# Performance work log

Hardware: AMD Instinct MI355X
Metric: run time of the kernel (lower is better)

## Reference

```python
import jax, jax.numpy as jnp
import numpy as np

SEQ_LEN = 1024
BATCH = 256
HIDDEN = 100
OUT = 1

L_FILTER = [-0.0106, 0.0329, 0.0308, -0.187, -0.028, 0.6309, 0.7148, 0.2304]
H_FILTER = [-0.2304, 0.7148, -0.6309, -0.028, 0.187, 0.0308, -0.0329, -0.0106]


def _create_W(P, is_l, rng):
    filt = L_FILTER if is_l else H_FILTER
    eps = np.min(np.abs(filt))
    W = rng.standard_normal((P, P)) * 0.1 * eps
    for i in range(P):
        for k, j in enumerate(range(i, min(i + len(filt), P))):
            W[i, j] = filt[k]
    return jnp.asarray(W, dtype=jnp.float32)


def setup_inputs() -> dict:
    key = jax.random.key(0)
    ks = jax.random.split(key, 16)
    rng = np.random.default_rng(0)
    T, H = SEQ_LEN, HIDDEN
    s = 1.0 / np.sqrt(H)

    def lstm_params(k):
        k1, k2, k3 = jax.random.split(k, 3)
        Wih = jax.random.uniform(k1, (4 * H, 1), jnp.float32, -s, s)
        Whh = jax.random.uniform(k2, (4 * H, H), jnp.float32, -s, s)
        b = jax.random.uniform(k3, (4 * H,), jnp.float32, -s, s)
        return Wih, Whh, b

    Wih1, Whh1, b1 = lstm_params(ks[0])
    Wih2, Whh2, b2 = lstm_params(ks[1])
    Wih3, Whh3, b3 = lstm_params(ks[2])
    return {
        "x": jax.random.normal(ks[3], (BATCH, T, 1), jnp.float32),
        "W1H": _create_W(T, False, rng),
        "b1H": jax.random.uniform(ks[4], (T,), jnp.float32, -1 / np.sqrt(T), 1 / np.sqrt(T)),
        "W1L": _create_W(T, True, rng),
        "b1L": jax.random.uniform(ks[5], (T,), jnp.float32, -1 / np.sqrt(T), 1 / np.sqrt(T)),
        "W2H": _create_W(T // 2, False, rng),
        "b2H": jax.random.uniform(ks[6], (T // 2,), jnp.float32, -1 / np.sqrt(T // 2), 1 / np.sqrt(T // 2)),
        "W2L": _create_W(T // 2, True, rng),
        "b2L": jax.random.uniform(ks[7], (T // 2,), jnp.float32, -1 / np.sqrt(T // 2), 1 / np.sqrt(T // 2)),
        "Wih1": Wih1, "Whh1": Whh1, "b1": b1,
        "Wih2": Wih2, "Whh2": Whh2, "b2": b2,
        "Wih3": Wih3, "Whh3": Whh3, "b3": b3,
        "Wout": jax.random.uniform(ks[8], (OUT, H), jnp.float32, -s, s),
        "bout": jax.random.uniform(ks[9], (OUT,), jnp.float32, -s, s),
    }


def _avgpool2(x):  # [B, L] -> [B, L//2], AvgPool1d(kernel=2, stride=2)
    B, L = x.shape
    return x.reshape(B, L // 2, 2).mean(-1)


def _lstm(x, Wih, Whh, b):
    # x: [B, T, 1]; torch LSTM gate order i, f, g, o; h0 = c0 = 0
    H = Whh.shape[1]
    gx = jnp.einsum('bti,gi->btg', x, Wih) + b  # [B, T, 4H]

    def step(carry, g):
        h, c = carry
        z = g + h @ Whh.T
        i, f, gg, o = jnp.split(z, 4, axis=-1)
        c = jax.nn.sigmoid(f) * c + jax.nn.sigmoid(i) * jnp.tanh(gg)
        h = jax.nn.sigmoid(o) * jnp.tanh(c)
        return (h, c), h

    B = x.shape[0]
    h0 = jnp.zeros((B, H), x.dtype)
    _, hs = jax.lax.scan(step, (h0, h0), jnp.swapaxes(gx, 0, 1))
    return jnp.swapaxes(hs, 0, 1)  # [B, T, H]


def reference(x, W1H, b1H, W1L, b1L, W2H, b2H, W2L, b2L,
              Wih1, Whh1, b1, Wih2, Whh2, b2, Wih3, Whh3, b3, Wout, bout):
    inp = x[:, :, -1]  # [B, T]
    ah1 = jax.nn.sigmoid(inp @ W1H.T + b1H)
    al1 = jax.nn.sigmoid(inp @ W1L.T + b1L)
    xh1 = _avgpool2(ah1)  # [B, T/2]
    xl1 = _avgpool2(al1)  # [B, T/2]
    ah2 = jax.nn.sigmoid(xl1 @ W2H.T + b2H)
    al2 = jax.nn.sigmoid(xl1 @ W2L.T + b2L)
    xh2 = _avgpool2(ah2)  # [B, T/4]
    xl2 = _avgpool2(al2)  # [B, T/4]
    s1 = _lstm(xh1[..., None], Wih1, Whh1, b1)
    s2 = _lstm(xh2[..., None], Wih2, Whh2, b2)
    s3 = _lstm(xl2[..., None], Wih3, Whh3, b3)
    cat = jnp.concatenate([s1, s2, s3], axis=1)  # [B, T, H]
    out = cat @ Wout.T + bout  # [B, T, OUT]
    return out[:, -1, :]
```

## Files before the change

kernel.cpp:

```cpp
#include <hip/hip_runtime.h>
#include <math.h>

typedef __bf16 bf16x8 __attribute__((ext_vector_type(8)));
typedef _Float16 f16x8 __attribute__((ext_vector_type(8)));
typedef _Float16 f16x4 __attribute__((ext_vector_type(4)));
typedef float f32x4 __attribute__((ext_vector_type(4)));

__device__ __forceinline__ unsigned short f2bf(float f) {
  unsigned int u = __builtin_bit_cast(unsigned int, f);
  u += 0x7fffu + ((u >> 16) & 1u);
  return (unsigned short)(u >> 16);
}
__device__ __forceinline__ unsigned int pack2bf(float a, float b) {
  return (unsigned int)f2bf(a) | ((unsigned int)f2bf(b) << 16);
}

#define GK_PADK 40
template <int WFP32, int XFP32>
__global__ __launch_bounds__(256) void gemm_mfma_sig_pool(
    const void* __restrict__ Wv, const float* __restrict__ bias,
    const void* __restrict__ Xv, void* __restrict__ Y,
    int K, int Np, int out_bf16) {
  __shared__ unsigned short Wt[64][GK_PADK];
  __shared__ unsigned short Xt[64][GK_PADK];
  const int tid = threadIdx.x;
  const int i_base = blockIdx.x * 64;
  const int b_base = blockIdx.y * 64;
  const int srow = tid >> 2, sseg = tid & 3;
  const int wv = tid >> 6, lane = tid & 63;
  const int wn = wv & 1, wb = wv >> 1;
  const int L15 = lane & 15, q = lane >> 4;

  f32x4 acc[2][2] = {};
  for (int k0 = 0; k0 < K; k0 += 32) {
    if (WFP32) {
      const float* Wf = (const float*)Wv;
      const float4 a = *(const float4*)&Wf[(size_t)(i_base + srow) * K + k0 + sseg * 8];
      const float4 b = *(const float4*)&Wf[(size_t)(i_base + srow) * K + k0 + sseg * 8 + 4];
      uint4 p = { pack2bf(a.x, a.y), pack2bf(a.z, a.w), pack2bf(b.x, b.y), pack2bf(b.z, b.w) };
      *(uint4*)&Wt[srow][sseg * 8] = p;
    } else {
      *(uint4*)&Wt[srow][sseg * 8] =
          *(const uint4*)&((const unsigned short*)Wv)[(size_t)(i_base + srow) * K + k0 + sseg * 8];
    }
    if (XFP32) {
      const float* Xf = (const float*)Xv;
      const float4 a = *(const float4*)&Xf[(size_t)(b_base + srow) * K + k0 + sseg * 8];
      const float4 b = *(const float4*)&Xf[(size_t)(b_base + srow) * K + k0 + sseg * 8 + 4];
      uint4 p = { pack2bf(a.x, a.y), pack2bf(a.z, a.w), pack2bf(b.x, b.y), pack2bf(b.z, b.w) };
      *(uint4*)&Xt[srow][sseg * 8] = p;
    } else {
      *(uint4*)&Xt[srow][sseg * 8] =
          *(const uint4*)&((const unsigned short*)Xv)[(size_t)(b_base + srow) * K + k0 + sseg * 8];
    }
    __syncthreads();
    bf16x8 a0 = *(const bf16x8*)&Wt[wn * 32 + L15][q * 8];
    bf16x8 a1 = *(const bf16x8*)&Wt[wn * 32 + 16 + L15][q * 8];
    bf16x8 b0 = *(const bf16x8*)&Xt[wb * 32 + L15][q * 8];
    bf16x8 b1 = *(const bf16x8*)&Xt[wb * 32 + 16 + L15][q * 8];
    acc[0][0] = __builtin_amdgcn_mfma_f32_16x16x32_bf16(a0, b0, acc[0][0], 0, 0, 0);
    acc[0][1] = __builtin_amdgcn_mfma_f32_16x16x32_bf16(a0, b1, acc[0][1], 0, 0, 0);
    acc[1][0] = __builtin_amdgcn_mfma_f32_16x16x32_bf16(a1, b0, acc[1][0], 0, 0, 0);
    acc[1][1] = __builtin_amdgcn_mfma_f32_16x16x32_bf16(a1, b1, acc[1][1], 0, 0, 0);
    __syncthreads();
  }

  const int nb0 = i_base + wn * 32;
  const int bc0 = b_base + wb * 32 + L15;
#pragma unroll
  for (int mg = 0; mg < 2; mg++) {
    const int nrow = nb0 + mg * 16 + q * 4;
    const float bi0 = bias[nrow], bi1 = bias[nrow + 1];
    const float bi2 = bias[nrow + 2], bi3 = bias[nrow + 3];
#pragma unroll
    for (int bg = 0; bg < 2; bg++) {
      const int b = bc0 + bg * 16;
      f32x4 A = acc[mg][bg];
      const float a0 = __builtin_amdgcn_rcpf(1.f + __expf(-(A[0] + bi0)));
      const float a1 = __builtin_amdgcn_rcpf(1.f + __expf(-(A[1] + bi1)));
      const float a2 = __builtin_amdgcn_rcpf(1.f + __expf(-(A[2] + bi2)));
      const float a3 = __builtin_amdgcn_rcpf(1.f + __expf(-(A[3] + bi3)));
      const float p0 = 0.5f * (a0 + a1), p1 = 0.5f * (a2 + a3);
      const int pidx = nrow >> 1;
      if (out_bf16) {
        *(unsigned int*)&((unsigned short*)Y)[(size_t)b * Np + pidx] = pack2bf(p0, p1);
      } else {
        *(float2*)&((float*)Y)[(size_t)b * Np + pidx] = make_float2(p0, p1);
      }
    }
  }
}

__global__ __launch_bounds__(256) void prep_whh(
    const float* __restrict__ Whh, const float* __restrict__ b3,
    _Float16* __restrict__ P) {
  const int idx = blockIdx.x * 256 + threadIdx.x;
  if (idx >= 400 * 16) return;
  const int row = idx >> 4, ch = idx & 15;
  const int hid = row >> 2, gate = row & 3;
  const int src = gate * 100 + hid;
  f16x8 v;
#pragma unroll
  for (int j = 0; j < 8; j++) {
    const int k = ch * 8 + j;
    float f = 0.f;
    if (k < 100) f = Whh[(size_t)src * 100 + k];
    v[j] = (_Float16)f;
  }
  *(f16x8*)&P[(size_t)row * 128 + ch * 8] = v;
}

#define TSTEPS 256

__device__ __forceinline__ float qb0(float x) {
  return __builtin_bit_cast(float, __builtin_amdgcn_mov_dpp(__builtin_bit_cast(int, x), 0x00, 0xf, 0xf, true));
}
__device__ __forceinline__ float qb1(float x) {
  return __builtin_bit_cast(float, __builtin_amdgcn_mov_dpp(__builtin_bit_cast(int, x), 0x55, 0xf, 0xf, true));
}
__device__ __forceinline__ float qb2(float x) {
  return __builtin_bit_cast(float, __builtin_amdgcn_mov_dpp(__builtin_bit_cast(int, x), 0xAA, 0xf, 0xf, true));
}
__device__ __forceinline__ float qb3(float x) {
  return __builtin_bit_cast(float, __builtin_amdgcn_mov_dpp(__builtin_bit_cast(int, x), 0xFF, 0xf, 0xf, true));
}

__global__ __launch_bounds__(512, 2) void lstm_mfma(
    const float* __restrict__ X, const _Float16* __restrict__ P,
    const float* __restrict__ Whh, const float* __restrict__ Wih,
    const float* __restrict__ b3, const float* __restrict__ Wout,
    const float* __restrict__ bout, float* __restrict__ out) {
  const int bat = blockIdx.x;
  const int t = threadIdx.x;
  const int w = t >> 6, lane = t & 63;
  const int quad = lane >> 4, c = lane & 15;
  const int TB = (w == 7) ? 21 : w * 3;
  const int NT = (w == 7) ? 4 : 3;

  __shared__ __align__(16) _Float16 hbuf[2][128];
  __shared__ float xrow[TSTEPS];
  __shared__ float red[128];

  for (int i = t; i < TSTEPS; i += 512) xrow[i] = X[(size_t)bat * TSTEPS + i];
  if (t < 128) { hbuf[0][t] = (_Float16)0.f; hbuf[1][t] = (_Float16)0.f; }

#define LDA(J, KT) const f16x8 A##J##KT = \
    *(const f16x8*)&P[(size_t)((TB + J) * 16 + c) * 128 + (KT) * 32 + quad * 8];
  LDA(0,0) LDA(0,1) LDA(0,2)
  LDA(1,0) LDA(1,1) LDA(1,2)
  LDA(2,0) LDA(2,1) LDA(2,2)
  LDA(3,0) LDA(3,1) LDA(3,2)
#undef LDA

  const bool act = (c < 4 * NT);
  const int J = c >> 2, g = c & 3;
  const int myhid = 4 * (TB + (act ? J : 0)) + quad;
  const int grow = g * 100 + myhid;
  const float u_ = Wih[grow];
  const float bz = b3[grow];
  const float4 wt = *(const float4*)&Whh[(size_t)grow * 100 + 96];
  const float kk = (g == 2) ? 2.f : 1.f;
  const float mm = (g == 2) ? 2.f : 1.f;
  const float dd = (g == 2) ? -1.f : 0.f;
  float cst = 0.f;
  __syncthreads();

#define SIG(zz) __builtin_amdgcn_rcpf(1.f + __expf(-(zz)))
#define STEPB(HC, HN, XT)                                                      \
  {                                                                            \
    const _Float16* hc = (HC);                                                 \
    const f16x8 B0 = *(const f16x8*)&hc[0 * 32 + quad * 8];                    \
    const f16x8 B1 = *(const f16x8*)&hc[1 * 32 + quad * 8];                    \
    const f16x8 B2 = *(const f16x8*)&hc[2 * 32 + quad * 8];                    \
    f32x4 z0 = {0.f,0.f,0.f,0.f}, z1 = z0, z2 = z0, z3 = z0;                   \
    { f32x4 za = z0, zb = z0;                                                  \
      za = __builtin_amdgcn_mfma_f32_16x16x32_f16(A00, B0, za, 0, 0, 0);       \
      zb = __builtin_amdgcn_mfma_f32_16x16x32_f16(A01, B1, zb, 0, 0, 0);       \
      za = __builtin_amdgcn_mfma_f32_16x16x32_f16(A02, B2, za, 0, 0, 0);       \
      z0 = za + zb; }                                                          \
    { f32x4 za = {0.f,0.f,0.f,0.f}, zb = za;                                   \
      za = __builtin_amdgcn_mfma_f32_16x16x32_f16(A10, B0, za, 0, 0, 0);       \
      zb = __builtin_amdgcn_mfma_f32_16x16x32_f16(A11, B1, zb, 0, 0, 0);       \
      za = __builtin_amdgcn_mfma_f32_16x16x32_f16(A12, B2, za, 0, 0, 0);       \
      z1 = za + zb; }                                                          \
    { f32x4 za = {0.f,0.f,0.f,0.f}, zb = za;                                   \
      za = __builtin_amdgcn_mfma_f32_16x16x32_f16(A20, B0, za, 0, 0, 0);       \
      zb = __builtin_amdgcn_mfma_f32_16x16x32_f16(A21, B1, zb, 0, 0, 0);       \
      za = __builtin_amdgcn_mfma_f32_16x16x32_f16(A22, B2, za, 0, 0, 0);       \
      z2 = za + zb; }                                                          \
    if (w == 7) {                                                              \
      f32x4 za = {0.f,0.f,0.f,0.f}, zb = za;                                   \
      za = __builtin_amdgcn_mfma_f32_16x16x32_f16(A30, B0, za, 0, 0, 0);       \
      zb = __builtin_amdgcn_mfma_f32_16x16x32_f16(A31, B1, zb, 0, 0, 0);       \
      za = __builtin_amdgcn_mfma_f32_16x16x32_f16(A32, B2, za, 0, 0, 0);       \
      z3 = za + zb; }                                                          \
    if (act) {                                                                 \
      const f32x4 zt = (J == 0) ? z0 : (J == 1) ? z1 : (J == 2) ? z2 : z3;     \
      float zs = (g == 0) ? zt[0] : (g == 1) ? zt[1] : (g == 2) ? zt[2] : zt[3];\
      const f16x4 ht = *(const f16x4*)&hc[96];                                 \
      zs = fmaf(wt.x, (float)ht[0], zs);                                       \
      zs = fmaf(wt.y, (float)ht[1], zs);                                       \
      zs = fmaf(wt.z, (float)ht[2], zs);                                       \
      zs = fmaf(wt.w, (float)ht[3], zs);                                       \
      zs = fmaf(u_, (XT), zs + bz);                                            \
      const float a = mm * SIG(kk * zs) + dd;                                  \
      const float ai = qb0(a), af = qb1(a), ag = qb2(a), ao = qb3(a);          \
      cst = fmaf(af, cst, ai * ag);                                            \
      const float th = 2.f * SIG(2.f * cst) - 1.f;                             \
      if (g == 0) (HN)[myhid] = (_Float16)(ao * th);                           \
    }                                                                          \
    __syncthreads();                                                           \
  }

  for (int step = 0; step < TSTEPS; step += 2) {
    STEPB(hbuf[0], hbuf[1], xrow[step]);
    STEPB(hbuf[1], hbuf[0], xrow[step + 1]);
  }
#undef STEPB
#undef SIG

  if (t < 128) {
    float a = 0.f;
    if (t < 100) a = (float)hbuf[0][t] * Wout[t];
    red[t] = a;
  }
  __syncthreads();
  if (t == 0) {
    float s = 0.f;
#pragma unroll
    for (int k = 0; k < 128; k++) s += red[k];
    out[bat] = s + bout[0];
  }
}

extern "C" void kernel_launch(void* const* d_in, const int* in_sizes, int n_in,
                              void* d_out, int out_size, void* d_ws, size_t ws_size,
                              hipStream_t stream) {
  const float* x    = (const float*)d_in[0];
  const float* W1L  = (const float*)d_in[3];
  const float* b1L  = (const float*)d_in[4];
  const float* W2L  = (const float*)d_in[7];
  const float* b2L  = (const float*)d_in[8];
  const float* Wih3 = (const float*)d_in[15];
  const float* Whh3 = (const float*)d_in[16];
  const float* b3   = (const float*)d_in[17];
  const float* Wout = (const float*)d_in[18];
  const float* bout = (const float*)d_in[19];
  float* out = (float*)d_out;

  unsigned short* xl1b = (unsigned short*)d_ws;
  float* xl2 = (float*)(xl1b + (size_t)256 * 512);
  _Float16* P = (_Float16*)(xl2 + (size_t)256 * 256);

  prep_whh<<<25, 256, 0, stream>>>(Whh3, b3, P);
  gemm_mfma_sig_pool<1, 1><<<dim3(16, 4), 256, 0, stream>>>(W1L, b1L, x, xl1b, 1024, 512, 1);
  gemm_mfma_sig_pool<1, 0><<<dim3(8, 4), 256, 0, stream>>>(W2L, b2L, xl1b, xl2, 512, 256, 0);
  lstm_mfma<<<256, 512, 0, stream>>>(xl2, P, Whh3, Wih3, b3, Wout, bout, out);
}
```

Baseline: 264.6 us.

## Halve LSTM block to four waves and pre-convert GEMM inputs to bf16

The LSTM recurrence kernel now runs each batch row with 256 threads (4 waves) instead of 512. Each wave computes 6–7 MFMA tiles and each lane handles two hidden-unit cell states, which cuts the cost of the per-step block barrier. The old Whh prep kernel is merged into a new conversion kernel that also casts W1L, W2L and x to bf16, so both GEMMs read bf16 operands directly. The trade-off is longer serial per-wave work per step and an extra full pass over the weights on every call.

```diff
diff --git a/kernel.cpp b/kernel.cpp
--- a/kernel.cpp
+++ b/kernel.cpp
@@ -13,6 +13,40 @@
 }
 __device__ __forceinline__ unsigned int pack2bf(float a, float b) {
   return (unsigned int)f2bf(a) | ((unsigned int)f2bf(b) << 16);
+}
+
+__global__ __launch_bounds__(256) void convert_prep(
+    const float* __restrict__ s0, const float* __restrict__ s1,
+    const float* __restrict__ s2, unsigned short* __restrict__ d0,
+    unsigned short* __restrict__ d1, unsigned short* __restrict__ d2,
+    int n0, int n1, int n2,
+    const float* __restrict__ Whh, _Float16* __restrict__ P) {
+  const int b = blockIdx.x;
+  if (b < 1536) {
+    int i4 = (b * 256 + threadIdx.x) * 4;
+    const float* s; unsigned short* d; int off;
+    if (i4 < n0) { s = s0; d = d0; off = i4; }
+    else if (i4 < n0 + n1) { s = s1; d = d1; off = i4 - n0; }
+    else if (i4 < n0 + n1 + n2) { s = s2; d = d2; off = i4 - n0 - n1; }
+    else return;
+    float4 v = *(const float4*)&s[off];
+    ushort4 o = { f2bf(v.x), f2bf(v.y), f2bf(v.z), f2bf(v.w) };
+    *(ushort4*)&d[off] = o;
+  } else {
+    const int idx = (b - 1536) * 256 + threadIdx.x;
+    if (idx >= 400 * 16) return;
+    const int row = idx >> 4, ch = idx & 15;
+    const int hid = row >> 2, gate = row & 3;
+    const int src = gate * 100 + hid;
+    f16x8 v;
+#pragma unroll
+    for (int j = 0; j < 8; j++) {
+      const int k = ch * 8 + j;
+      float f = (k < 100) ? Whh[(size_t)src * 100 + k] : 0.f;
+      v[j] = (_Float16)f;
+    }
+    *(f16x8*)&P[(size_t)row * 128 + ch * 8] = v;
+  }
 }
 
 #define GK_PADK 40
@@ -91,25 +125,6 @@
   }
 }
 
-__global__ __launch_bounds__(256) void prep_whh(
-    const float* __restrict__ Whh, const float* __restrict__ b3,
-    _Float16* __restrict__ P) {
-  const int idx = blockIdx.x * 256 + threadIdx.x;
-  if (idx >= 400 * 16) return;
-  const int row = idx >> 4, ch = idx & 15;
-  const int hid = row >> 2, gate = row & 3;
-  const int src = gate * 100 + hid;
-  f16x8 v;
-#pragma unroll
-  for (int j = 0; j < 8; j++) {
-    const int k = ch * 8 + j;
-    float f = 0.f;
-    if (k < 100) f = Whh[(size_t)src * 100 + k];
-    v[j] = (_Float16)f;
-  }
-  *(f16x8*)&P[(size_t)row * 128 + ch * 8] = v;
-}
-
 #define TSTEPS 256
 
 __device__ __forceinline__ float qb0(float x) {
@@ -125,7 +140,7 @@
   return __builtin_bit_cast(float, __builtin_amdgcn_mov_dpp(__builtin_bit_cast(int, x), 0xFF, 0xf, 0xf, true));
 }
 
-__global__ __launch_bounds__(512, 2) void lstm_mfma(
+__global__ __launch_bounds__(256, 1) void lstm_mfma(
     const float* __restrict__ X, const _Float16* __restrict__ P,
     const float* __restrict__ Whh, const float* __restrict__ Wih,
     const float* __restrict__ b3, const float* __restrict__ Wout,
@@ -134,15 +149,15 @@
   const int t = threadIdx.x;
   const int w = t >> 6, lane = t & 63;
   const int quad = lane >> 4, c = lane & 15;
-  const int TB = (w == 7) ? 21 : w * 3;
-  const int NT = (w == 7) ? 4 : 3;
+  const int TB = (w == 3) ? 18 : w * 6;
+  const int NT = (w == 3) ? 7 : 6;
 
   __shared__ __align__(16) _Float16 hbuf[2][128];
   __shared__ float xrow[TSTEPS];
   __shared__ float red[128];
 
-  for (int i = t; i < TSTEPS; i += 512) xrow[i] = X[(size_t)bat * TSTEPS + i];
-  if (t < 128) { hbuf[0][t] = (_Float16)0.f; hbuf[1][t] = (_Float16)0.f; }
+  for (int i = t; i < TSTEPS; i += 256) xrow[i] = X[(size_t)bat * TSTEPS + i];
+  ((_Float16*)hbuf)[t] = (_Float16)0.f;
 
 #define LDA(J, KT) const f16x8 A##J##KT = \
     *(const f16x8*)&P[(size_t)((TB + J) * 16 + c) * 128 + (KT) * 32 + quad * 8];
@@ -150,19 +165,26 @@
   LDA(1,0) LDA(1,1) LDA(1,2)
   LDA(2,0) LDA(2,1) LDA(2,2)
   LDA(3,0) LDA(3,1) LDA(3,2)
+  LDA(4,0) LDA(4,1) LDA(4,2)
+  LDA(5,0) LDA(5,1) LDA(5,2)
+  LDA(6,0) LDA(6,1) LDA(6,2)
 #undef LDA
 
-  const bool act = (c < 4 * NT);
-  const int J = c >> 2, g = c & 3;
-  const int myhid = 4 * (TB + (act ? J : 0)) + quad;
-  const int grow = g * 100 + myhid;
-  const float u_ = Wih[grow];
-  const float bz = b3[grow];
-  const float4 wt = *(const float4*)&Whh[(size_t)grow * 100 + 96];
+  const int g = c & 3, ssel = c >> 2;
+  const int sB = 4 + ssel;
+  const bool actB = (sB < NT);
+  const int hidA = 4 * (TB + ssel) + quad;
+  const int hidB = 4 * (TB + (actB ? sB : 0)) + quad;
+  const int growA = g * 100 + hidA;
+  const int growB = g * 100 + hidB;
+  const float uA = Wih[growA], bzA = b3[growA];
+  const float uB = Wih[growB], bzB = b3[growB];
+  const float4 wtA = *(const float4*)&Whh[(size_t)growA * 100 + 96];
+  const float4 wtB = *(const float4*)&Whh[(size_t)growB * 100 + 96];
   const float kk = (g == 2) ? 2.f : 1.f;
   const float mm = (g == 2) ? 2.f : 1.f;
   const float dd = (g == 2) ? -1.f : 0.f;
-  float cst = 0.f;
+  float cstA = 0.f, cstB = 0.f;
   __syncthreads();
 
 #define SIG(zz) __builtin_amdgcn_rcpf(1.f + __expf(-(zz)))
@@ -173,41 +195,58 @@
     const f16x8 B1 = *(const f16x8*)&hc[1 * 32 + quad * 8];                    \
     const f16x8 B2 = *(const f16x8*)&hc[2 * 32 + quad * 8];                    \
     f32x4 z0 = {0.f,0.f,0.f,0.f}, z1 = z0, z2 = z0, z3 = z0;                   \
-    { f32x4 za = z0, zb = z0;                                                  \
-      za = __builtin_amdgcn_mfma_f32_16x16x32_f16(A00, B0, za, 0, 0, 0);       \
-      zb = __builtin_amdgcn_mfma_f32_16x16x32_f16(A01, B1, zb, 0, 0, 0);       \
-      za = __builtin_amdgcn_mfma_f32_16x16x32_f16(A02, B2, za, 0, 0, 0);       \
-      z0 = za + zb; }                                                          \
-    { f32x4 za = {0.f,0.f,0.f,0.f}, zb = za;                                   \
-      za = __builtin_amdgcn_mfma_f32_16x16x32_f16(A10, B0, za, 0, 0, 0);       \
-      zb = __builtin_amdgcn_mfma_f32_16x16x32_f16(A11, B1, zb, 0, 0, 0);       \
-      za = __builtin_amdgcn_mfma_f32_16x16x32_f16(A12, B2, za, 0, 0, 0);       \
-      z1 = za + zb; }                                                          \
-    { f32x4 za = {0.f,0.f,0.f,0.f}, zb = za;                                   \
-      za = __builtin_amdgcn_mfma_f32_16x16x32_f16(A20, B0, za, 0, 0, 0);       \
-      zb = __builtin_amdgcn_mfma_f32_16x16x32_f16(A21, B1, zb, 0, 0, 0);       \
-      za = __builtin_amdgcn_mfma_f32_16x16x32_f16(A22, B2, za, 0, 0, 0);       \
-      z2 = za + zb; }                                                          \
-    if (w == 7) {                                                              \
-      f32x4 za = {0.f,0.f,0.f,0.f}, zb = za;                                   \
-      za = __builtin_amdgcn_mfma_f32_16x16x32_f16(A30, B0, za, 0, 0, 0);       \
-      zb = __builtin_amdgcn_mfma_f32_16x16x32_f16(A31, B1, zb, 0, 0, 0);       \
-      za = __builtin_amdgcn_mfma_f32_16x16x32_f16(A32, B2, za, 0, 0, 0);       \
-      z3 = za + zb; }                                                          \
-    if (act) {                                                                 \
-      const f32x4 zt = (J == 0) ? z0 : (J == 1) ? z1 : (J == 2) ? z2 : z3;     \
-      float zs = (g == 0) ? zt[0] : (g == 1) ? zt[1] : (g == 2) ? zt[2] : zt[3];\
-      const f16x4 ht = *(const f16x4*)&hc[96];                                 \
-      zs = fmaf(wt.x, (float)ht[0], zs);                                       \
-      zs = fmaf(wt.y, (float)ht[1], zs);                                       \
-      zs = fmaf(wt.z, (float)ht[2], zs);                                       \
-      zs = fmaf(wt.w, (float)ht[3], zs);                                       \
-      zs = fmaf(u_, (XT), zs + bz);                                            \
-      const float a = mm * SIG(kk * zs) + dd;                                  \
-      const float ai = qb0(a), af = qb1(a), ag = qb2(a), ao = qb3(a);          \
-      cst = fmaf(af, cst, ai * ag);                                            \
-      const float th = 2.f * SIG(2.f * cst) - 1.f;                             \
-      if (g == 0) (HN)[myhid] = (_Float16)(ao * th);                           \
+    f32x4 z4 = z0, z5 = z0, z6 = z0;                                           \
+    z0 = __builtin_amdgcn_mfma_f32_16x16x32_f16(A00, B0, z0, 0, 0, 0);         \
+    z0 = __builtin_amdgcn_mfma_f32_16x16x32_f16(A01, B1, z0, 0, 0, 0);         \
+    z0 = __builtin_amdgcn_mfma_f32_16x16x32_f16(A02, B2, z0, 0, 0, 0);         \
+    z1 = __builtin_amdgcn_mfma_f32_16x16x32_f16(A10, B0, z1, 0, 0, 0);         \
+    z1 = __builtin_amdgcn_mfma_f32_16x16x32_f16(A11, B1, z1, 0, 0, 0);         \
+    z1 = __builtin_amdgcn_mfma_f32_16x16x32_f16(A12, B2, z1, 0, 0, 0);         \
+    z2 = __builtin_amdgcn_mfma_f32_16x16x32_f16(A20, B0, z2, 0, 0, 0);         \
+    z2 = __builtin_amdgcn_mfma_f32_16x16x32_f16(A21, B1, z2, 0, 0, 0);         \
+    z2 = __builtin_amdgcn_mfma_f32_16x16x32_f16(A22, B2, z2, 0, 0, 0);         \
+    z3 = __builtin_amdgcn_mfma_f32_16x16x32_f16(A30, B0, z3, 0, 0, 0);         \
+    z3 = __builtin_amdgcn_mfma_f32_16x16x32_f16(A31, B1, z3, 0, 0, 0);         \
+    z3 = __builtin_amdgcn_mfma_f32_16x16x32_f16(A32, B2, z3, 0, 0, 0);         \
+    z4 = __builtin_amdgcn_mfma_f32_16x16x32_f16(A40, B0, z4, 0, 0, 0);         \
+    z4 = __builtin_amdgcn_mfma_f32_16x16x32_f16(A41, B1, z4, 0, 0, 0);         \
+    z4 = __builtin_amdgcn_mfma_f32_16x16x32_f16(A42, B2, z4, 0, 0, 0);         \
+    z5 = __builtin_amdgcn_mfma_f32_16x16x32_f16(A50, B0, z5, 0, 0, 0);         \
+    z5 = __builtin_amdgcn_mfma_f32_16x16x32_f16(A51, B1, z5, 0, 0, 0);         \
+    z5 = __builtin_amdgcn_mfma_f32_16x16x32_f16(A52, B2, z5, 0, 0, 0);         \
+    if (w == 3) {                                                              \
+      z6 = __builtin_amdgcn_mfma_f32_16x16x32_f16(A60, B0, z6, 0, 0, 0);       \
+      z6 = __builtin_amdgcn_mfma_f32_16x16x32_f16(A61, B1, z6, 0, 0, 0);       \
+      z6 = __builtin_amdgcn_mfma_f32_16x16x32_f16(A62, B2, z6, 0, 0, 0);       \
+    }                                                                          \
+    const f16x4 htv = *(const f16x4*)&hc[96];                                  \
+    const float h96 = (float)htv[0], h97 = (float)htv[1];                      \
+    const float h98 = (float)htv[2], h99 = (float)htv[3];                      \
+    const f32x4 ztA = (ssel == 0) ? z0 : (ssel == 1) ? z1 : (ssel == 2) ? z2 : z3; \
+    const f32x4 ztB = (ssel == 0) ? z4 : (ssel == 1) ? z5 : z6;                \
+    float zsA = (g == 0) ? ztA[0] : (g == 1) ? ztA[1] : (g == 2) ? ztA[2] : ztA[3]; \
+    float zsB = (g == 0) ? ztB[0] : (g == 1) ? ztB[1] : (g == 2) ? ztB[2] : ztB[3]; \
+    {                                                                          \
+      float zz = zsA;                                                          \
+      zz = fmaf(wtA.x, h96, zz); zz = fmaf(wtA.y, h97, zz);                    \
+      zz = fmaf(wtA.z, h98, zz); zz = fmaf(wtA.w, h99, zz);                    \
+      zz = fmaf(uA, (XT), zz + bzA);                                           \
+      const float a = mm * SIG(kk * zz) + dd;                                  \
+      const float ai = qb0(a), af = qb1(a), ag2 = qb2(a), ao = qb3(a);         \
+      cstA = fmaf(af, cstA, ai * ag2);                                         \
+      const float th = 2.f * SIG(2.f * cstA) - 1.f;                            \
+      if (g == 0) (HN)[hidA] = (_Float16)(ao * th);                            \
+    }                                                                          \
+    {                                                                          \
+      float zz = zsB;                                                          \
+      zz = fmaf(wtB.x, h96, zz); zz = fmaf(wtB.y, h97, zz);                    \
+      zz = fmaf(wtB.z, h98, zz); zz = fmaf(wtB.w, h99, zz);                    \
+      zz = fmaf(uB, (XT), zz + bzB);                                           \
+      const float a = mm * SIG(kk * zz) + dd;                                  \
+      const float ai = qb0(a), af = qb1(a), ag2 = qb2(a), ao = qb3(a);         \
+      cstB = fmaf(af, cstB, ai * ag2);                                         \
+      const float th = 2.f * SIG(2.f * cstB) - 1.f;                            \
+      if (actB && g == 0) (HN)[hidB] = (_Float16)(ao * th);                    \
     }                                                                          \
     __syncthreads();                                                           \
   }
@@ -248,12 +287,16 @@
   const float* bout = (const float*)d_in[19];
   float* out = (float*)d_out;
 
-  unsigned short* xl1b = (unsigned short*)d_ws;
-  float* xl2 = (float*)(xl1b + (size_t)256 * 512);
-  _Float16* P = (_Float16*)(xl2 + (size_t)256 * 256);
-
-  prep_whh<<<25, 256, 0, stream>>>(Whh3, b3, P);
-  gemm_mfma_sig_pool<1, 1><<<dim3(16, 4), 256, 0, stream>>>(W1L, b1L, x, xl1b, 1024, 512, 1);
-  gemm_mfma_sig_pool<1, 0><<<dim3(8, 4), 256, 0, stream>>>(W2L, b2L, xl1b, xl2, 512, 256, 0);
-  lstm_mfma<<<256, 512, 0, stream>>>(xl2, P, Whh3, Wih3, b3, Wout, bout, out);
-}
+  unsigned short* W1Lb = (unsigned short*)d_ws;
+  unsigned short* W2Lb = W1Lb + 1048576;
+  unsigned short* xb   = W2Lb + 262144;
+  unsigned short* xl1b = xb + 262144;
+  float* xl2 = (float*)(xl1b + 131072);
+  _Float16* P = (_Float16*)(xl2 + 65536);
+
+  convert_prep<<<1561, 256, 0, stream>>>(W1L, W2L, x, W1Lb, W2Lb, xb,
+                                         1048576, 262144, 262144, Whh3, P);
+  gemm_mfma_sig_pool<0, 0><<<dim3(16, 4), 256, 0, stream>>>(W1Lb, b1L, xb, xl1b, 1024, 512, 1);
+  gemm_mfma_sig_pool<0, 0><<<dim3(8, 4), 256, 0, stream>>>(W2Lb, b2L, xl1b, xl2, 512, 256, 0);
+  lstm_mfma<<<256, 256, 0, stream>>>(xl2, P, Whh3, Wih3, b3, Wout, bout, out);
+}
```

After: 264.7 us. No clear change (+0.0%).
